# Kernel optimization log

Hardware: AMD Instinct MI355X
Metric: run time of the kernel (lower is better)

## Reference

```python
import jax, jax.numpy as jnp
import numpy as np


def _backwarp(img, flow):
    """Bilinear backward warp of img [B,C,H,W] by flow [B,2,H,W] (pixels).
    Matches torch grid_sample(mode='bilinear', padding_mode='zeros', align_corners=False)
    with the standard softmax-splatting backwarp grid construction."""
    B, C, H, W = img.shape
    # normalized base grid (align_corners=False convention used by backwarp)
    hor = jnp.linspace(-1.0 + 1.0 / W, 1.0 - 1.0 / W, W, dtype=img.dtype)  # [W]
    ver = jnp.linspace(-1.0 + 1.0 / H, 1.0 - 1.0 / H, H, dtype=img.dtype)  # [H]
    gx = hor[None, None, :] + flow[:, 0] / ((W - 1.0) / 2.0)  # [B,H,W]
    gy = ver[None, :, None] + flow[:, 1] / ((H - 1.0) / 2.0)  # [B,H,W]
    # unnormalize (align_corners=False): x = ((g+1)*size - 1)/2
    ix = ((gx + 1.0) * W - 1.0) * 0.5
    iy = ((gy + 1.0) * H - 1.0) * 0.5
    x0 = jnp.floor(ix)
    y0 = jnp.floor(iy)
    wx1 = ix - x0
    wy1 = iy - y0
    wx0 = 1.0 - wx1
    wy0 = 1.0 - wy1

    flat = img.reshape(B, C, H * W)

    def gather(xi, yi):
        valid = (xi >= 0) & (xi <= W - 1) & (yi >= 0) & (yi <= H - 1)  # [B,H,W]
        xc = jnp.clip(xi, 0, W - 1).astype(jnp.int32)
        yc = jnp.clip(yi, 0, H - 1).astype(jnp.int32)
        idx = (yc * W + xc).reshape(B, 1, H * W)
        v = jnp.take_along_axis(flat, jnp.broadcast_to(idx, (B, C, H * W)), axis=2)
        return v.reshape(B, C, H, W) * valid[:, None].astype(img.dtype)

    x1 = x0 + 1.0
    y1 = y0 + 1.0
    out = (gather(x0, y0) * (wy0 * wx0)[:, None]
           + gather(x1, y0) * (wy0 * wx1)[:, None]
           + gather(x0, y1) * (wy1 * wx0)[:, None]
           + gather(x1, y1) * (wy1 * wx1)[:, None])
    return out


def setup_inputs() -> dict:
    key = jax.random.key(0)
    k1, k2, k3 = jax.random.split(key, 3)
    B, C, H, W = 16, 3, 768, 1024
    ten_first = jax.random.normal(k1, (B, C, H, W), dtype=jnp.float32)
    ten_second = jax.random.normal(k2, (B, C, H, W), dtype=jnp.float32)
    tenFlow = jax.random.normal(k3, (B, 2, H, W), dtype=jnp.float32)
    alpha = -jnp.ones((1, 1, 1, 1), dtype=jnp.float32)  # learnable scale, init -1
    return {"ten_first": ten_first, "ten_second": ten_second, "tenFlow": tenFlow, "alpha": alpha}


def reference(ten_first, ten_second, tenFlow, alpha):
    warped = _backwarp(ten_second, tenFlow)
    l1 = jnp.abs(ten_first - warped)                       # [B,C,H,W]
    return alpha * jnp.mean(l1, axis=1, keepdims=True)     # [B,1,H,W]
```

## Files before the change

kernel.cpp:

```cpp
#include <hip/hip_runtime.h>

constexpr int B  = 16;
constexpr int C  = 3;
constexpr int H  = 768;
constexpr int W  = 1024;
constexpr int HW = H * W;

__global__ __launch_bounds__(256) void warp_l1_mean_kernel(
    const float* __restrict__ first,
    const float* __restrict__ second,
    const float* __restrict__ flow,
    const float* __restrict__ alpha,
    float* __restrict__ out)
{
    const int gid = blockIdx.x * blockDim.x + threadIdx.x;
    if (gid >= B * HW) return;

    const int b = gid / HW;
    const int p = gid - b * HW;
    const int y = p / W;
    const int x = p - y * W;

    const float* fl = flow + (size_t)b * 2 * HW;
    const float fx = fl[p];
    const float fy = fl[HW + p];

    const float ix = (float)x + fx * ((float)W / (float)(W - 1));
    const float iy = (float)y + fy * ((float)H / (float)(H - 1));

    const float x0f = floorf(ix);
    const float y0f = floorf(iy);
    const float wx1 = ix - x0f;
    const float wy1 = iy - y0f;
    const float wx0 = 1.0f - wx1;
    const float wy0 = 1.0f - wy1;

    const int x0 = (int)x0f;
    const int y0 = (int)y0f;
    const int x1 = x0 + 1;
    const int y1 = y0 + 1;

    const bool vx0 = (x0 >= 0) && (x0 <= W - 1);
    const bool vx1 = (x1 >= 0) && (x1 <= W - 1);
    const bool vy0 = (y0 >= 0) && (y0 <= H - 1);
    const bool vy1 = (y1 >= 0) && (y1 <= H - 1);

    const int cx0 = min(max(x0, 0), W - 1);
    const int cx1 = min(max(x1, 0), W - 1);
    const int cy0 = min(max(y0, 0), H - 1);
    const int cy1 = min(max(y1, 0), H - 1);

    const float w00 = wy0 * wx0 * ((vx0 && vy0) ? 1.0f : 0.0f);
    const float w01 = wy0 * wx1 * ((vx1 && vy0) ? 1.0f : 0.0f);
    const float w10 = wy1 * wx0 * ((vx0 && vy1) ? 1.0f : 0.0f);
    const float w11 = wy1 * wx1 * ((vx1 && vy1) ? 1.0f : 0.0f);

    const int i00 = cy0 * W + cx0;
    const int i01 = cy0 * W + cx1;
    const int i10 = cy1 * W + cx0;
    const int i11 = cy1 * W + cx1;

    const float* sec = second + (size_t)b * C * HW;
    const float* fst = first  + (size_t)b * C * HW;
    const float a = alpha[0];

    float acc = 0.0f;
#pragma unroll
    for (int c = 0; c < C; ++c) {
        const float* s = sec + c * HW;
        const float warped = w00 * s[i00] + w01 * s[i01]
                           + w10 * s[i10] + w11 * s[i11];
        acc += fabsf(fst[c * HW + p] - warped);
    }

    out[gid] = a * (acc * (1.0f / 3.0f));
}

extern "C" void kernel_launch(void* const* d_in, const int* in_sizes, int n_in,
                              void* d_out, int out_size, void* d_ws, size_t ws_size,
                              hipStream_t stream) {
    const float* first  = (const float*)d_in[0];
    const float* second = (const float*)d_in[1];
    const float* flow   = (const float*)d_in[2];
    const float* alpha  = (const float*)d_in[3];
    float* out = (float*)d_out;

    const int total = B * HW;
    const int block = 256;
    const int grid  = (total + block - 1) / block;

    warp_l1_mean_kernel<<<grid, block, 0, stream>>>(first, second, flow, alpha, out);
}
```

Measured before the change: 408.1 us.

## Process four pixels per thread with vectorized streaming loads and paired-texel gathers

Each thread now handles four consecutive pixels. Flow, first-image and output traffic goes through 128-bit nontemporal loads and stores. The four bilinear taps are fetched as two 2-float loads per row, using a clamped base column and select offsets, which halves the gather instruction count. A 2D grid removes the integer division used for batch and pixel indexing. The cost is higher register pressure and fewer threads in flight for the latency-bound random gathers.

```diff
diff --git a/kernel.cpp b/kernel.cpp
--- a/kernel.cpp
+++ b/kernel.cpp
@@ -6,74 +6,94 @@
 constexpr int W  = 1024;
 constexpr int HW = H * W;
 
-__global__ __launch_bounds__(256) void warp_l1_mean_kernel(
+typedef float f2 __attribute__((ext_vector_type(2), aligned(4)));
+typedef float f4 __attribute__((ext_vector_type(4)));
+
+__global__ __launch_bounds__(256) void warp_l1_mean_v2(
     const float* __restrict__ first,
     const float* __restrict__ second,
     const float* __restrict__ flow,
     const float* __restrict__ alpha,
     float* __restrict__ out)
 {
-    const int gid = blockIdx.x * blockDim.x + threadIdx.x;
-    if (gid >= B * HW) return;
+    const int b = blockIdx.y;
+    const int p = (blockIdx.x * 256 + (int)threadIdx.x) * 4;
+    const int y  = p >> 10;
+    const int xb = p & (W - 1);
 
-    const int b = gid / HW;
-    const int p = gid - b * HW;
-    const int y = p / W;
-    const int x = p - y * W;
+    const float* fl  = flow   + (size_t)b * 2 * HW;
+    const float* fst = first  + (size_t)b * C * HW;
+    const float* sec = second + (size_t)b * C * HW;
 
-    const float* fl = flow + (size_t)b * 2 * HW;
-    const float fx = fl[p];
-    const float fy = fl[HW + p];
+    const f4 fx = __builtin_nontemporal_load((const f4*)(fl + p));
+    const f4 fy = __builtin_nontemporal_load((const f4*)(fl + HW + p));
 
-    const float ix = (float)x + fx * ((float)W / (float)(W - 1));
-    const float iy = (float)y + fy * ((float)H / (float)(H - 1));
+    int   row0[4], row1[4];
+    int   off0[4], off1[4];
+    float hx0[4], hx1[4], gy0[4], gy1[4];
 
-    const float x0f = floorf(ix);
-    const float y0f = floorf(iy);
-    const float wx1 = ix - x0f;
-    const float wy1 = iy - y0f;
-    const float wx0 = 1.0f - wx1;
-    const float wy0 = 1.0f - wy1;
+#pragma unroll
+    for (int i = 0; i < 4; ++i) {
+        const float ix = (float)(xb + i) + fx[i] * ((float)W / (float)(W - 1));
+        const float iy = (float)y        + fy[i] * ((float)H / (float)(H - 1));
+        const float x0f = floorf(ix);
+        const float y0f = floorf(iy);
+        const float wx1 = ix - x0f;
+        const float wy1 = iy - y0f;
 
-    const int x0 = (int)x0f;
-    const int y0 = (int)y0f;
-    const int x1 = x0 + 1;
-    const int y1 = y0 + 1;
+        const int x0  = (int)x0f;
+        const int y0i = (int)y0f;
+        const int x1  = x0 + 1;
+        const int y1  = y0i + 1;
 
-    const bool vx0 = (x0 >= 0) && (x0 <= W - 1);
-    const bool vx1 = (x1 >= 0) && (x1 <= W - 1);
-    const bool vy0 = (y0 >= 0) && (y0 <= H - 1);
-    const bool vy1 = (y1 >= 0) && (y1 <= H - 1);
+        const int bx = min(max(x0, 0), W - 2);
+        off0[i] = min(max(x0 - bx, 0), 1);
+        off1[i] = min(max(x1 - bx, 0), 1);
 
-    const int cx0 = min(max(x0, 0), W - 1);
-    const int cx1 = min(max(x1, 0), W - 1);
-    const int cy0 = min(max(y0, 0), H - 1);
-    const int cy1 = min(max(y1, 0), H - 1);
+        const float vx0 = ((unsigned)x0  < (unsigned)W) ? 1.0f : 0.0f;
+        const float vx1 = ((unsigned)x1  < (unsigned)W) ? 1.0f : 0.0f;
+        const float vy0 = ((unsigned)y0i < (unsigned)H) ? 1.0f : 0.0f;
+        const float vy1 = ((unsigned)y1  < (unsigned)H) ? 1.0f : 0.0f;
 
-    const float w00 = wy0 * wx0 * ((vx0 && vy0) ? 1.0f : 0.0f);
-    const float w01 = wy0 * wx1 * ((vx1 && vy0) ? 1.0f : 0.0f);
-    const float w10 = wy1 * wx0 * ((vx0 && vy1) ? 1.0f : 0.0f);
-    const float w11 = wy1 * wx1 * ((vx1 && vy1) ? 1.0f : 0.0f);
+        hx0[i] = (1.0f - wx1) * vx0;
+        hx1[i] = wx1 * vx1;
+        gy0[i] = (1.0f - wy1) * vy0;
+        gy1[i] = wy1 * vy1;
 
-    const int i00 = cy0 * W + cx0;
-    const int i01 = cy0 * W + cx1;
-    const int i10 = cy1 * W + cx0;
-    const int i11 = cy1 * W + cx1;
+        const int cy0 = min(max(y0i, 0), H - 1);
+        const int cy1 = min(max(y1,  0), H - 1);
+        row0[i] = cy0 * W + bx;
+        row1[i] = cy1 * W + bx;
+    }
 
-    const float* sec = second + (size_t)b * C * HW;
-    const float* fst = first  + (size_t)b * C * HW;
-    const float a = alpha[0];
+    const f4 a0 = __builtin_nontemporal_load((const f4*)(fst + p));
+    const f4 a1 = __builtin_nontemporal_load((const f4*)(fst + HW + p));
+    const f4 a2 = __builtin_nontemporal_load((const f4*)(fst + 2 * HW + p));
 
-    float acc = 0.0f;
+    f4 acc = {0.0f, 0.0f, 0.0f, 0.0f};
+
 #pragma unroll
     for (int c = 0; c < C; ++c) {
         const float* s = sec + c * HW;
-        const float warped = w00 * s[i00] + w01 * s[i01]
-                           + w10 * s[i10] + w11 * s[i11];
-        acc += fabsf(fst[c * HW + p] - warped);
+#pragma unroll
+        for (int i = 0; i < 4; ++i) {
+            const f2 v0 = *(const f2*)(s + row0[i]);
+            const f2 v1 = *(const f2*)(s + row1[i]);
+            const float t00 = off0[i] ? v0.y : v0.x;
+            const float t01 = off1[i] ? v0.y : v0.x;
+            const float t10 = off0[i] ? v1.y : v1.x;
+            const float t11 = off1[i] ? v1.y : v1.x;
+            const float warped = gy0[i] * (hx0[i] * t00 + hx1[i] * t01)
+                               + gy1[i] * (hx0[i] * t10 + hx1[i] * t11);
+            const float af = (c == 0) ? a0[i] : (c == 1) ? a1[i] : a2[i];
+            acc[i] += fabsf(af - warped);
+        }
     }
 
-    out[gid] = a * (acc * (1.0f / 3.0f));
+    const float s = alpha[0] * (1.0f / 3.0f);
+    f4 r;
+    r.x = acc.x * s; r.y = acc.y * s; r.z = acc.z * s; r.w = acc.w * s;
+    __builtin_nontemporal_store(r, (f4*)(out + (size_t)b * HW + p));
 }
 
 extern "C" void kernel_launch(void* const* d_in, const int* in_sizes, int n_in,
@@ -85,9 +105,6 @@
     const float* alpha  = (const float*)d_in[3];
     float* out = (float*)d_out;
 
-    const int total = B * HW;
-    const int block = 256;
-    const int grid  = (total + block - 1) / block;
-
-    warp_l1_mean_kernel<<<grid, block, 0, stream>>>(first, second, flow, alpha, out);
+    dim3 grid(HW / (4 * 256), B);
+    warp_l1_mean_v2<<<grid, dim3(256), 0, stream>>>(first, second, flow, alpha, out);
 }
```

Measured after the change: 452.9 us. +11.0%, slower.
